# Performance work log

Hardware: AMD Instinct MI355X
Metric: run time of the kernel (lower is better)

## Reference

```python
import jax, jax.numpy as jnp
import numpy as np
from jax.scipy.special import logsumexp

T = 2_000_000
NTAGS = 5
START, STOP = 3, 4
NEG = -10000.0


def setup_inputs() -> dict:
    key = jax.random.key(0)
    k1, k2, k3 = jax.random.split(key, 3)
    feats = jax.random.normal(k1, (T, NTAGS), dtype=jnp.float32)
    tags = jax.random.randint(k2, (T,), 0, 3, dtype=jnp.int32)
    transitions = jax.random.normal(k3, (NTAGS, NTAGS), dtype=jnp.float32)
    # transitions[START, :] = -10000 ; transitions[:, STOP] = -10000
    transitions = transitions.at[START, :].set(NEG).at[:, STOP].set(NEG)
    return {"feats": feats, "tags": tags, "transitions": transitions}


def reference(feats, tags, transitions):
    # ---- forward algorithm (log partition) ----
    init = jnp.full((NTAGS,), NEG, dtype=feats.dtype).at[START].set(0.0)

    def step(fv, feat):
        # new[next] = LSE_prev( fv[prev] + transitions[next, prev] + feat[next] )
        nv = logsumexp(fv[None, :] + transitions, axis=1) + feat
        return nv, None

    fv, _ = jax.lax.scan(step, init, feats)
    alpha = logsumexp(fv + transitions[STOP])

    # ---- gold path score ----
    tags_ext = jnp.concatenate([jnp.array([START], dtype=tags.dtype), tags])
    prev_t, next_t = tags_ext[:-1], tags_ext[1:]
    trans_score = jnp.sum(transitions[next_t, prev_t])
    emit_score = jnp.sum(jnp.take_along_axis(feats, next_t[:, None].astype(jnp.int32), axis=1))
    gold = trans_score + emit_score + transitions[STOP, tags_ext[-1]]

    return alpha - gold
```

## Files before the change

kernel.cpp:

```cpp
#include <hip/hip_runtime.h>

#define T_LEN     2000000
#define NT        5
#define START_TAG 3
#define STOP_TAG  4
#define CH        8
#define BTHR      256
#define NBLK      1024
#define SPB       (BTHR * CH)
#define GOFF      (NBLK * 13)
#define ID_OFF    (-1.0e30f)
#define FSTR      25

__device__ __forceinline__ void compose13(const float* L, const float* R, float* C) {
    float t[12];
#pragma unroll
    for (int j = 0; j < 3; ++j)
#pragma unroll
        for (int s = 0; s < 4; ++s)
            t[j * 4 + s] = fmaf(L[j * 4 + 0], R[0 * 4 + s],
                           fmaf(L[j * 4 + 1], R[1 * 4 + s],
                                L[j * 4 + 2] * R[2 * 4 + s]));
    float m = t[0];
#pragma unroll
    for (int k = 1; k < 12; ++k) m = fmaxf(m, t[k]);
    const float r    = 1.0f / m;
    const float toff = L[12] + R[12] + __logf(m);
    const bool  Lid  = L[12] < -1e29f;
    const bool  Rid  = R[12] < -1e29f;
#pragma unroll
    for (int k = 0; k < 12; ++k)
        C[k] = Rid ? L[k] : (Lid ? R[k] : t[k] * r);
    C[12] = Rid ? L[12] : (Lid ? R[12] : toff);
}

__global__ __launch_bounds__(BTHR) void crf_phase1(
    const float* __restrict__ feats, const int* __restrict__ tags,
    const float* __restrict__ trans, float* __restrict__ ws)
{
    __shared__ __align__(16) char smem[BTHR * FSTR * 4 + BTHR * 9 * 4];
    __shared__ float sTr[NT * NT];

    float* sF  = (float*)smem;
    int*   sTg = (int*)(smem + BTHR * FSTR * 4);

    const int tid = threadIdx.x;
    if (tid < NT * NT) sTr[tid] = trans[tid];

    const long blockBase = (long)blockIdx.x * SPB;

    {
        const float* gF   = feats + blockBase * NT;
        const long   remL = (long)T_LEN * NT - blockBase * NT;
        const int    remF = (int)(remL < 0 ? 0 : (remL > SPB * NT ? SPB * NT : remL));
#pragma unroll
        for (int k = 0; k < 10; ++k) {
            const int dw = (tid + k * BTHR) * 4;
            if (dw < remF) {
                const float4 v = *(const float4*)(gF + dw);
                const float vv[4] = {v.x, v.y, v.z, v.w};
#pragma unroll
                for (int e = 0; e < 4; ++e) {
                    const int x    = dw + e;
                    const int step = x / 5;
                    const int c    = x - step * 5;
                    if (c < 3)
                        sF[(step >> 3) * FSTR + (step & 7) * 3 + c] = vv[e];
                }
            }
        }
    }
    {
        const int* gT   = tags + blockBase;
        const long remL = (long)T_LEN - blockBase;
        const int  remT = (int)(remL < 0 ? 0 : (remL > SPB ? SPB : remL));
#pragma unroll
        for (int k = 0; k < 2; ++k) {
            const int idx = (tid + k * BTHR) * 4;
            if (idx < remT) {
                const int4 v = *(const int4*)(gT + idx);
                int* d = sTg + (idx >> 3) * 9 + (idx & 7);
                d[0] = v.x; d[1] = v.y; d[2] = v.z; d[3] = v.w;
            }
        }
    }
    __syncthreads();

    const long start  = blockBase + (long)tid * CH;
    const bool active = (start < T_LEN);

    float A[12];
    float off  = ID_OFF;
    float gold = 0.0f;

    if (active) {
        float E[12];
#pragma unroll
        for (int j = 0; j < 3; ++j)
#pragma unroll
            for (int s = 0; s < 4; ++s)
                E[j * 4 + s] = __expf(sTr[j * NT + s]);

        const float* myF = sF + tid * FSTR;
        const int*   myT = sTg + tid * 9;

        int prev;
        if (tid > 0)            prev = sTg[(tid - 1) * 9 + (CH - 1)];
        else if (blockIdx.x)    prev = tags[start - 1];
        else                    prev = START_TAG;

        {
            const float f0 = myF[0], f1 = myF[1], f2 = myF[2];
            const float e0 = __expf(f0), e1 = __expf(f1), e2 = __expf(f2);
#pragma unroll
            for (int s = 0; s < 4; ++s) {
                A[0 * 4 + s] = e0 * E[0 * 4 + s];
                A[1 * 4 + s] = e1 * E[1 * 4 + s];
                A[2 * 4 + s] = e2 * E[2 * 4 + s];
            }
            const int tg = myT[0];
            gold = sTr[tg * NT + prev] + (tg == 0 ? f0 : (tg == 1 ? f1 : f2));
            prev = tg;
        }
#pragma unroll
        for (int t = 1; t < CH; ++t) {
            const float f0 = myF[t * 3 + 0], f1 = myF[t * 3 + 1], f2 = myF[t * 3 + 2];
            const float e0 = __expf(f0), e1 = __expf(f1), e2 = __expf(f2);
            float N[12];
#pragma unroll
            for (int s = 0; s < 4; ++s) {
                const float a0 = A[0 * 4 + s], a1 = A[1 * 4 + s], a2 = A[2 * 4 + s];
                N[0 * 4 + s] = e0 * fmaf(E[0], a0, fmaf(E[1], a1, E[2] * a2));
                N[1 * 4 + s] = e1 * fmaf(E[4], a0, fmaf(E[5], a1, E[6] * a2));
                N[2 * 4 + s] = e2 * fmaf(E[8], a0, fmaf(E[9], a1, E[10] * a2));
            }
#pragma unroll
            for (int k = 0; k < 12; ++k) A[k] = N[k];

            const int tg = myT[t];
            gold += sTr[tg * NT + prev] + (tg == 0 ? f0 : (tg == 1 ? f1 : f2));
            prev = tg;
        }
        float m = A[0];
#pragma unroll
        for (int k = 1; k < 12; ++k) m = fmaxf(m, A[k]);
        const float r = 1.0f / m;
#pragma unroll
        for (int k = 0; k < 12; ++k) A[k] *= r;
        off = __logf(m);

        if (start + CH == T_LEN) gold += sTr[STOP_TAG * NT + prev];
    } else {
#pragma unroll
        for (int k = 0; k < 12; ++k) A[k] = 0.0f;
    }

    __syncthreads();
    float* sM = (float*)smem;
    float* sG = (float*)(smem + BTHR * 13 * 4);

#pragma unroll
    for (int k = 0; k < 12; ++k) sM[tid * 13 + k] = A[k];
    sM[tid * 13 + 12] = off;
    sG[tid]           = gold;
    __syncthreads();

    for (int h = BTHR / 2; h >= 1; h >>= 1) {
        float C[13];
        float gg = 0.0f;
        const bool act = (tid < h);
        if (act) {
            float L[13], R[13];
#pragma unroll
            for (int k = 0; k < 13; ++k) {
                L[k] = sM[(2 * tid + 1) * 13 + k];
                R[k] = sM[(2 * tid) * 13 + k];
            }
            compose13(L, R, C);
            gg = sG[2 * tid] + sG[2 * tid + 1];
        }
        __syncthreads();
        if (act) {
#pragma unroll
            for (int k = 0; k < 13; ++k) sM[tid * 13 + k] = C[k];
            sG[tid] = gg;
        }
        __syncthreads();
    }

    if (tid < 13) ws[blockIdx.x * 13 + tid] = sM[tid];
    if (tid == 0) ws[GOFF + blockIdx.x] = sG[0];
}

__global__ __launch_bounds__(256) void crf_phase2(
    const float* __restrict__ trans, const float* __restrict__ ws,
    float* __restrict__ out)
{
    __shared__ float sM[256 * 13];
    __shared__ float sG[256];

    const int tid = threadIdx.x;

    {
        float acc[13], nxt[13], C[13];
#pragma unroll
        for (int k = 0; k < 13; ++k) acc[k] = ws[(4 * tid) * 13 + k];
        float gg = ws[GOFF + 4 * tid];
#pragma unroll
        for (int g = 1; g < 4; ++g) {
#pragma unroll
            for (int k = 0; k < 13; ++k) nxt[k] = ws[(4 * tid + g) * 13 + k];
            compose13(nxt, acc, C);
#pragma unroll
            for (int k = 0; k < 13; ++k) acc[k] = C[k];
            gg += ws[GOFF + 4 * tid + g];
        }
#pragma unroll
        for (int k = 0; k < 13; ++k) sM[tid * 13 + k] = acc[k];
        sG[tid] = gg;
    }
    __syncthreads();

    for (int h = 128; h >= 1; h >>= 1) {
        float C[13];
        float gg = 0.0f;
        const bool act = (tid < h);
        if (act) {
            float L[13], R[13];
#pragma unroll
            for (int k = 0; k < 13; ++k) {
                L[k] = sM[(2 * tid + 1) * 13 + k];
                R[k] = sM[(2 * tid) * 13 + k];
            }
            compose13(L, R, C);
            gg = sG[2 * tid] + sG[2 * tid + 1];
        }
        __syncthreads();
        if (act) {
#pragma unroll
            for (int k = 0; k < 13; ++k) sM[tid * 13 + k] = C[k];
            sG[tid] = gg;
        }
        __syncthreads();
    }

    if (tid == 0) {
        float s = 0.0f;
#pragma unroll
        for (int j = 0; j < 3; ++j)
            s += sM[j * 4 + 3] * __expf(trans[STOP_TAG * NT + j]);
        const float alpha = sM[12] + __logf(s);
        out[0] = alpha - sG[0];
    }
}

extern "C" void kernel_launch(void* const* d_in, const int* in_sizes, int n_in,
                              void* d_out, int out_size, void* d_ws, size_t ws_size,
                              hipStream_t stream) {
    const float* feats = (const float*)d_in[0];
    const int*   tags  = (const int*)d_in[1];
    const float* trans = (const float*)d_in[2];
    float*       out   = (float*)d_out;
    float*       ws    = (float*)d_ws;

    crf_phase1<<<NBLK, BTHR, 0, stream>>>(feats, tags, trans, ws);
    crf_phase2<<<1, 256, 0, stream>>>(trans, ws, out);
}
```

Before: 98.81 us.

## Fuse phase kernels via last-block atomic and replace LDS tree with wave shuffles

Merges the two kernels into one. Each block publishes its partial result and increments an atomic counter, and the last block to finish performs the final reduction. The in-block reduction now has 64 threads each fold four partials serially, then finish with a wavefront shuffle-xor tree, instead of a shared-memory tree with a barrier per level. This removes a kernel launch and several barriers, but adds a memset launch, a threadfence and an atomic, plus a serialized final reduction inside the last block.

```diff
diff --git a/kernel.cpp b/kernel.cpp
--- a/kernel.cpp
+++ b/kernel.cpp
@@ -9,6 +9,7 @@
 #define NBLK      1024
 #define SPB       (BTHR * CH)
 #define GOFF      (NBLK * 13)
+#define CNT_OFF   (NBLK * 14)
 #define ID_OFF    (-1.0e30f)
 #define FSTR      25
 
@@ -34,12 +35,29 @@
     C[12] = Rid ? L[12] : (Lid ? R[12] : toff);
 }
 
-__global__ __launch_bounds__(BTHR) void crf_phase1(
+__device__ __forceinline__ void wave_tree(float* acc, float& g, int lane) {
+#pragma unroll
+    for (int d = 1; d < 64; d <<= 1) {
+        float P[13], C[13];
+#pragma unroll
+        for (int k = 0; k < 13; ++k) P[k] = __shfl_xor(acc[k], d, 64);
+        const float gp = __shfl_xor(g, d, 64);
+        if (lane & d) compose13(acc, P, C);
+        else          compose13(P, acc, C);
+#pragma unroll
+        for (int k = 0; k < 13; ++k) acc[k] = C[k];
+        g += gp;
+    }
+}
+
+__global__ __launch_bounds__(BTHR, 4) void crf_fused(
     const float* __restrict__ feats, const int* __restrict__ tags,
-    const float* __restrict__ trans, float* __restrict__ ws)
+    const float* __restrict__ trans, float* __restrict__ ws,
+    float* __restrict__ out)
 {
     __shared__ __align__(16) char smem[BTHR * FSTR * 4 + BTHR * 9 * 4];
     __shared__ float sTr[NT * NT];
+    __shared__ int   sLast;
 
     float* sF  = (float*)smem;
     int*   sTg = (int*)(smem + BTHR * FSTR * 4);
@@ -165,92 +183,81 @@
     sG[tid]           = gold;
     __syncthreads();
 
-    for (int h = BTHR / 2; h >= 1; h >>= 1) {
-        float C[13];
-        float gg = 0.0f;
-        const bool act = (tid < h);
-        if (act) {
-            float L[13], R[13];
-#pragma unroll
-            for (int k = 0; k < 13; ++k) {
-                L[k] = sM[(2 * tid + 1) * 13 + k];
-                R[k] = sM[(2 * tid) * 13 + k];
-            }
-            compose13(L, R, C);
-            gg = sG[2 * tid] + sG[2 * tid + 1];
-        }
+    if (tid < 64) {
+        float acc[13];
+#pragma unroll
+        for (int k = 0; k < 13; ++k) acc[k] = sM[(4 * tid) * 13 + k];
+        float g = sG[4 * tid];
+#pragma unroll
+        for (int q = 1; q < 4; ++q) {
+            float nxt[13], C[13];
+#pragma unroll
+            for (int k = 0; k < 13; ++k) nxt[k] = sM[(4 * tid + q) * 13 + k];
+            compose13(nxt, acc, C);
+#pragma unroll
+            for (int k = 0; k < 13; ++k) acc[k] = C[k];
+            g += sG[4 * tid + q];
+        }
+        wave_tree(acc, g, tid);
+
+        if (tid == 0) {
+#pragma unroll
+            for (int k = 0; k < 13; ++k) ws[blockIdx.x * 13 + k] = acc[k];
+            ws[GOFF + blockIdx.x] = g;
+            __threadfence();
+            const int old = atomicAdd((int*)(ws + CNT_OFF), 1);
+            sLast = (old == NBLK - 1) ? 1 : 0;
+        }
+    }
+    __syncthreads();
+
+    if (sLast) {
+        __threadfence();
+        float acc[13];
+#pragma unroll
+        for (int k = 0; k < 13; ++k) acc[k] = ws[(4 * tid) * 13 + k];
+        float g = ws[GOFF + 4 * tid];
+#pragma unroll
+        for (int q = 1; q < 4; ++q) {
+            float nxt[13], C[13];
+#pragma unroll
+            for (int k = 0; k < 13; ++k) nxt[k] = ws[(4 * tid + q) * 13 + k];
+            compose13(nxt, acc, C);
+#pragma unroll
+            for (int k = 0; k < 13; ++k) acc[k] = C[k];
+            g += ws[GOFF + 4 * tid + q];
+        }
+#pragma unroll
+        for (int k = 0; k < 13; ++k) sM[tid * 13 + k] = acc[k];
+        sG[tid] = g;
         __syncthreads();
-        if (act) {
-#pragma unroll
-            for (int k = 0; k < 13; ++k) sM[tid * 13 + k] = C[k];
-            sG[tid] = gg;
-        }
-        __syncthreads();
-    }
-
-    if (tid < 13) ws[blockIdx.x * 13 + tid] = sM[tid];
-    if (tid == 0) ws[GOFF + blockIdx.x] = sG[0];
-}
-
-__global__ __launch_bounds__(256) void crf_phase2(
-    const float* __restrict__ trans, const float* __restrict__ ws,
-    float* __restrict__ out)
-{
-    __shared__ float sM[256 * 13];
-    __shared__ float sG[256];
-
-    const int tid = threadIdx.x;
-
-    {
-        float acc[13], nxt[13], C[13];
-#pragma unroll
-        for (int k = 0; k < 13; ++k) acc[k] = ws[(4 * tid) * 13 + k];
-        float gg = ws[GOFF + 4 * tid];
-#pragma unroll
-        for (int g = 1; g < 4; ++g) {
-#pragma unroll
-            for (int k = 0; k < 13; ++k) nxt[k] = ws[(4 * tid + g) * 13 + k];
-            compose13(nxt, acc, C);
-#pragma unroll
-            for (int k = 0; k < 13; ++k) acc[k] = C[k];
-            gg += ws[GOFF + 4 * tid + g];
-        }
-#pragma unroll
-        for (int k = 0; k < 13; ++k) sM[tid * 13 + k] = acc[k];
-        sG[tid] = gg;
-    }
-    __syncthreads();
-
-    for (int h = 128; h >= 1; h >>= 1) {
-        float C[13];
-        float gg = 0.0f;
-        const bool act = (tid < h);
-        if (act) {
-            float L[13], R[13];
-#pragma unroll
-            for (int k = 0; k < 13; ++k) {
-                L[k] = sM[(2 * tid + 1) * 13 + k];
-                R[k] = sM[(2 * tid) * 13 + k];
-            }
-            compose13(L, R, C);
-            gg = sG[2 * tid] + sG[2 * tid + 1];
-        }
-        __syncthreads();
-        if (act) {
-#pragma unroll
-            for (int k = 0; k < 13; ++k) sM[tid * 13 + k] = C[k];
-            sG[tid] = gg;
-        }
-        __syncthreads();
-    }
-
-    if (tid == 0) {
-        float s = 0.0f;
-#pragma unroll
-        for (int j = 0; j < 3; ++j)
-            s += sM[j * 4 + 3] * __expf(trans[STOP_TAG * NT + j]);
-        const float alpha = sM[12] + __logf(s);
-        out[0] = alpha - sG[0];
+
+        if (tid < 64) {
+            float a2[13];
+#pragma unroll
+            for (int k = 0; k < 13; ++k) a2[k] = sM[(4 * tid) * 13 + k];
+            float gg = sG[4 * tid];
+#pragma unroll
+            for (int q = 1; q < 4; ++q) {
+                float nxt[13], C[13];
+#pragma unroll
+                for (int k = 0; k < 13; ++k) nxt[k] = sM[(4 * tid + q) * 13 + k];
+                compose13(nxt, a2, C);
+#pragma unroll
+                for (int k = 0; k < 13; ++k) a2[k] = C[k];
+                gg += sG[4 * tid + q];
+            }
+            wave_tree(a2, gg, tid);
+
+            if (tid == 0) {
+                float s = 0.0f;
+#pragma unroll
+                for (int j = 0; j < 3; ++j)
+                    s += a2[j * 4 + 3] * __expf(sTr[STOP_TAG * NT + j]);
+                const float alpha = a2[12] + __logf(s);
+                out[0] = alpha - gg;
+            }
+        }
     }
 }
 
@@ -263,6 +270,6 @@
     float*       out   = (float*)d_out;
     float*       ws    = (float*)d_ws;
 
-    crf_phase1<<<NBLK, BTHR, 0, stream>>>(feats, tags, trans, ws);
-    crf_phase2<<<1, 256, 0, stream>>>(trans, ws, out);
-}
+    hipMemsetAsync((char*)d_ws + CNT_OFF * 4, 0, 4, stream);
+    crf_fused<<<NBLK, BTHR, 0, stream>>>(feats, tags, trans, ws, out);
+}
```

Result: slower. 120.5 us (+21.9%).
